# Kernel tuning notes

Hardware: AMD Instinct MI355X
Metric: run time of the kernel (lower is better)

The kernel has to match this reference:

```python
import jax, jax.numpy as jnp
import numpy as np

DEPTH = 256
SEQ = 394
EMB = 300


def _branch(x_nch, W, b, n):
    # W: [depth, n*EMB], flatten order of paragraph[i:i+n,:].flatten() is (time, emb)
    k = W.reshape(DEPTH, n, EMB).transpose(0, 2, 1)  # OIH: [depth, EMB, n]
    y = jax.lax.conv_general_dilated(
        x_nch, k, window_strides=(1,), padding='VALID',
        dimension_numbers=('NCH', 'OIH', 'NCH'))  # [B, depth, SEQ-n+1]
    # original loop only covers windows i = 0 .. SEQ-n-1 (SEQ-n windows)
    y = y[:, :, :SEQ - n] + b  # b: [depth, 1] broadcasts over time
    # running max starts at 0 and relu clamps >= 0; outer relu is a no-op
    return jnp.max(jax.nn.relu(y), axis=-1)  # [B, depth]


def setup_inputs() -> dict:
    key = jax.random.key(0)
    ks = jax.random.split(key, 7)
    inp = {
        'input': jax.random.normal(ks[0], (64, SEQ, EMB), dtype=jnp.float32),
        'W1': jax.random.normal(ks[1], (DEPTH, 3 * EMB), dtype=jnp.float32),
        'W2': jax.random.normal(ks[2], (DEPTH, 4 * EMB), dtype=jnp.float32),
        'W3': jax.random.normal(ks[3], (DEPTH, 5 * EMB), dtype=jnp.float32),
        'b1': jax.random.normal(ks[4], (DEPTH, 1), dtype=jnp.float32),
        'b2': jax.random.normal(ks[5], (DEPTH, 1), dtype=jnp.float32),
        'b3': jax.random.normal(ks[6], (DEPTH, 1), dtype=jnp.float32),
    }
    return inp


def reference(input, W1, W2, W3, b1, b2, b3):
    x = input.transpose(0, 2, 1)  # [B, EMB, SEQ] (NCH)
    o1 = _branch(x, W1, b1, 3)
    o2 = _branch(x, W2, b2, 4)
    o3 = _branch(x, W3, b3, 5)
    return jnp.concatenate([o1, o2, o3], axis=1)  # [B, 3*depth]
```

## Files before the change

kernel.cpp:

```cpp
#include <hip/hip_runtime.h>
#include <hip/hip_bf16.h>

#define SEQ 394
#define EMB 300
#define EMBP 312
#define NROWS (64 * SEQ)
#define NCHT 118
#define CBE0 29
#define CBE1 68
#define XROWS 69
#define XGR 2691
#define XELEM 21528

typedef __attribute__((ext_vector_type(8))) short short8;
typedef __attribute__((ext_vector_type(4))) float f32x4;

__device__ __forceinline__ unsigned short f2b(float f) {
    unsigned u = __float_as_uint(f);
    u += 0x7FFFu + ((u >> 16) & 1u);
    return (unsigned short)(u >> 16);
}


__global__ __launch_bounds__(256)
void pack_w_kernel(const float* __restrict__ W1, const float* __restrict__ W2,
                   const float* __restrict__ W3, unsigned short* __restrict__ wb)
{
    int G = blockIdx.x * 256 + threadIdx.x;
    int l  = G & 63;
    int g  = (G >> 6) & 15;
    int c  = G >> 10;
    const float* Wg; int n, cb;
    if (c <= CBE0)      { Wg = W1; n = 3; cb = 0;        }
    else if (c <= CBE1) { Wg = W2; n = 4; cb = CBE0 + 1; }
    else                { Wg = W3; n = 5; cb = CBE1 + 1; }
    const int K = n * 300;
    const int f = g * 16 + (l & 15);
    const int kl = (c - cb) * 32 + (l >> 4) * 8;
    unsigned short v[8];
#pragma unroll
    for (int j = 0; j < 8; ++j) {
        int kk = kl + j;
        int r  = kk / EMBP;
        int e  = kk - r * EMBP;
        v[j] = (r < n && e < 300) ? f2b(Wg[(long)f * K + r * 300 + e]) : (unsigned short)0;
    }
    unsigned short* dst = wb + (long)G * 8;
    *(ushort4*)dst       = make_ushort4(v[0], v[1], v[2], v[3]);
    *(ushort4*)(dst + 4) = make_ushort4(v[4], v[5], v[6], v[7]);
}


__global__ __launch_bounds__(512, 4)
void convgemm_kernel(const float* __restrict__ x,
                     const unsigned short* __restrict__ wb,
                     const float* __restrict__ b1, const float* __restrict__ b2,
                     const float* __restrict__ b3,
                     float* __restrict__ out)
{
    __shared__ unsigned short X[XELEM];

    const int tid  = threadIdx.x;
    const int lane = tid & 63;
    const int wfs  = tid >> 6;
    const int lr   = lane & 15, lg = lane >> 4;
    const int b    = blockIdx.x >> 3;
    const int ti   = blockIdx.x & 7;
    const int woff = ti * 49;

    const unsigned short* wp0 = wb + ((long)(wfs * 2) * 64 + lane) * 8;
    auto LDW = [&](int c, short8 (&w)[2]) {
        const short8* p = (const short8*)(wp0 + (long)c * 8192);
        w[0] = p[0];
        w[1] = p[64];
    };

    short8 w1[2], w2[2];
    LDW(30, w1); LDW(69, w2);

    {
        const float* xs = x + ((long)b * SEQ + woff) * 300;
        const long growbase = (long)b * SEQ + woff;
#pragma unroll
        for (int rd = 0; rd < 6; ++rd) {
            int gi = rd * 512 + tid;
            if (gi < XGR) {
                int row = gi / 39;
                int g   = gi - row * 39;
                const float* src = xs + (long)gi * 8 - 12 * row;
                float4 v0 = make_float4(0.f, 0.f, 0.f, 0.f);
                float4 v1 = make_float4(0.f, 0.f, 0.f, 0.f);
                if (growbase + row < NROWS) {
                    if (g < 37) {
                        v0 = *(const float4*)src;
                        v1 = *(const float4*)(src + 4);
                    } else if (g == 37) {
                        v0 = *(const float4*)src;
                    }
                }
                short8 s;
                s[0] = (short)f2b(v0.x); s[1] = (short)f2b(v0.y);
                s[2] = (short)f2b(v0.z); s[3] = (short)f2b(v0.w);
                s[4] = (short)f2b(v1.x); s[5] = (short)f2b(v1.y);
                s[6] = (short)f2b(v1.z); s[7] = (short)f2b(v1.w);
                *(short8*)&X[gi * 8] = s;
            }
        }
    }
    __syncthreads();

    const unsigned short* xr = &X[lr * EMBP + lg * 8];
    auto RDBX = [&](int ko, short8 (&bx)[4]) {
        bx[0] = *(const short8*)(xr + ko);
        bx[1] = *(const short8*)(xr + ko + 16 * EMBP);
        bx[2] = *(const short8*)(xr + ko + 32 * EMBP);
        bx[3] = *(const short8*)(xr + ko + 48 * EMBP);
    };

    auto MFMA8 = [&](const short8 (&w)[2], const short8 (&bx)[4], f32x4 (&acc)[2][4]) {
#pragma unroll
        for (int mi = 0; mi < 2; ++mi)
#pragma unroll
            for (int ni = 0; ni < 4; ++ni)
                acc[mi][ni] = __builtin_amdgcn_mfma_f32_16x16x32_bf16(w[mi], bx[ni], acc[mi][ni], 0, 0, 0);
    };

    auto EPI = [&](int br, f32x4 (&acc)[2][4]) {
        const float* bg = (br == 0) ? b1 : (br == 1) ? b2 : b3;
        const int Nw = 391 - br;
        const int ob = b * 768 + br * 256;
#pragma unroll
        for (int mi = 0; mi < 2; ++mi) {
#pragma unroll
            for (int r = 0; r < 4; ++r) {
                const int d = wfs * 32 + mi * 16 + lg * 4 + r;
                const float bv = bg[d];
                float m = 0.f;
#pragma unroll
                for (int ni = 0; ni < 4; ++ni) {
                    int w = woff + ni * 16 + lr;
                    float v = fmaxf(acc[mi][ni][r] + bv, 0.f);
                    if (w >= Nw) v = 0.f;
                    m = fmaxf(m, v);
                }
#pragma unroll
                for (int off = 1; off < 16; off <<= 1)
                    m = fmaxf(m, __shfl_xor(m, off));
                if (lr == 0)
                    atomicMax((int*)(out + ob + d), __float_as_int(m));
            }
        }
#pragma unroll
        for (int i = 0; i < 2; ++i)
#pragma unroll
            for (int j = 0; j < 4; ++j)
                acc[i][j] = (f32x4)0.0f;
    };

    f32x4 accA[2][4], accB[2][4];
#pragma unroll
    for (int i = 0; i < 2; ++i)
#pragma unroll
        for (int j = 0; j < 4; ++j) {
            accA[i][j] = (f32x4)0.0f;
            accB[i][j] = (f32x4)0.0f;
        }

    short8 bxA[4], bxB[4];
    RDBX(0, bxA);

    for (int j = 0; j < 38; j += 2) {
        RDBX((j + 1) * 32, bxB);
        MFMA8(w1, bxA, accA);
        MFMA8(w2, bxA, accB);
        LDW(30 + j + 1, w1); LDW(69 + j + 1, w2);

        RDBX((j + 2) * 32, bxA);
        MFMA8(w1, bxB, accA);
        MFMA8(w2, bxB, accB);
        LDW(30 + j + 2, w1); LDW(69 + j + 2, w2);
    }
    MFMA8(w1, bxA, accA);
    MFMA8(w2, bxA, accB);

    LDW(108, w2);
    RDBX(39 * 32, bxB);
    EPI(1, accA);

    for (int u = 0; u < 10; u += 2) {
        RDBX((40 + u) * 32, bxA);
        MFMA8(w2, bxB, accB);
        LDW(109 + u, w2);

        { int t = (41 + u <= 48) ? 41 + u : 48; RDBX(t * 32, bxB); }
        MFMA8(w2, bxA, accB);
        { int t = (110 + u <= 117) ? 110 + u : 117; LDW(t, w2); }
    }

    LDW(0, w1);
    RDBX(0, bxA);
    EPI(2, accB);

    for (int j = 0; j < 30; j += 2) {
        RDBX((j + 1) * 32, bxB);
        MFMA8(w1, bxA, accA);
        LDW(j + 1, w1);

        { int t = (j + 2 <= 29) ? j + 2 : 29; RDBX(t * 32, bxA); }
        MFMA8(w1, bxB, accA);
        { int t = (j + 2 <= 29) ? j + 2 : 29; LDW(t, w1); }
    }
    EPI(0, accA);
}


__device__ __forceinline__ void load_chunk(const float* __restrict__ Wg,
                                           const float* __restrict__ xb,
                                           int K, int dbase, int i0, int k0, int tid,
                                           float4 wv[4], float4 xv[4])
{
#pragma unroll
    for (int i = 0; i < 4; ++i) {
        int fi  = tid + (i << 8);
        int row = fi >> 3;
        int c4  = (fi & 7) << 2;
        int col = k0 + c4;
        if (col < K)
            wv[i] = *(const float4*)(Wg + (long)(dbase + row) * K + col);
        else
            wv[i] = make_float4(0.f, 0.f, 0.f, 0.f);
        int off = (i0 + row) * EMB + col;
        int lim = SEQ * EMB - 4;
        if (off > lim) off = lim;
        xv[i] = *(const float4*)(xb + off);
    }
}

__device__ __forceinline__ void write_chunk(unsigned short (*Wb)[40],
                                            unsigned short (*Xb)[40],
                                            int tid, const float4 wv[4], const float4 xv[4])
{
#pragma unroll
    for (int i = 0; i < 4; ++i) {
        int fi  = tid + (i << 8);
        int row = fi >> 3;
        int c4  = (fi & 7) << 2;
        *(ushort4*)&Wb[row][c4] = make_ushort4(f2b(wv[i].x), f2b(wv[i].y), f2b(wv[i].z), f2b(wv[i].w));
        *(ushort4*)&Xb[row][c4] = make_ushort4(f2b(xv[i].x), f2b(xv[i].y), f2b(xv[i].z), f2b(xv[i].w));
    }
}

__global__ __launch_bounds__(256, 2)
void convmax_fallback(const float* __restrict__ x,
                      const float* __restrict__ W1, const float* __restrict__ W2,
                      const float* __restrict__ W3,
                      const float* __restrict__ b1, const float* __restrict__ b2,
                      const float* __restrict__ b3,
                      float* __restrict__ out)
{
    const int br = blockIdx.z;
    const int K  = (br == 0) ? 900 : (br == 1) ? 1200 : 1500;
    const int Nw = SEQ - 3 - br;
    const float* Wg = (br == 0) ? W1 : (br == 1) ? W2 : W3;
    const float* bg = (br == 0) ? b1 : (br == 1) ? b2 : b3;
    const int b  = blockIdx.x;
    const int mt = blockIdx.y >> 2;
    const int nt = blockIdx.y & 3;
    const int dbase = mt * 128;
    const int i0    = nt * 128;
    const float* xb = x + b * (SEQ * EMB);
    const int nch = (K + 31) >> 5;

    __shared__ unsigned short Wl[2][128][40];
    __shared__ unsigned short Xl[2][128][40];

    const int tid  = threadIdx.x;
    const int lane = tid & 63;
    const int wid  = tid >> 6;
    const int wr = wid >> 1, wc = wid & 1;
    const int lr = lane & 15, lg = lane >> 4;

    f32x4 acc[4][4];
#pragma unroll
    for (int i = 0; i < 4; ++i)
#pragma unroll
        for (int j = 0; j < 4; ++j)
            acc[i][j] = (f32x4)0.0f;

    {
        float4 wv[4], xv[4];
        load_chunk(Wg, xb, K, dbase, i0, 0, tid, wv, xv);
        write_chunk(Wl[0], Xl[0], tid, wv, xv);
    }
    __syncthreads();

    for (int c = 0; c < nch; ++c) {
        const int cur = c & 1;
        float4 wv[4], xv[4];
        const bool pf = (c + 1 < nch);
        if (pf) load_chunk(Wg, xb, K, dbase, i0, (c + 1) << 5, tid, wv, xv);

        short8 af[4], bfr[4];
#pragma unroll
        for (int mi = 0; mi < 4; ++mi)
            af[mi] = *(const short8*)&Wl[cur][wr * 64 + mi * 16 + lr][lg * 8];
#pragma unroll
        for (int ni = 0; ni < 4; ++ni)
            bfr[ni] = *(const short8*)&Xl[cur][wc * 64 + ni * 16 + lr][lg * 8];
#pragma unroll
        for (int mi = 0; mi < 4; ++mi)
#pragma unroll
            for (int ni = 0; ni < 4; ++ni)
                acc[mi][ni] = __builtin_amdgcn_mfma_f32_16x16x32_bf16(af[mi], bfr[ni], acc[mi][ni], 0, 0, 0);

        if (pf) write_chunk(Wl[cur ^ 1], Xl[cur ^ 1], tid, wv, xv);
        __syncthreads();
    }

    const int ob = b * 768 + br * 256;
#pragma unroll
    for (int mi = 0; mi < 4; ++mi) {
#pragma unroll
        for (int rI = 0; rI < 4; ++rI) {
            const int d = dbase + wr * 64 + mi * 16 + lg * 4 + rI;
            const float bv = bg[d];
            float m = 0.f;
#pragma unroll
            for (int ni = 0; ni < 4; ++ni) {
                int win = i0 + wc * 64 + ni * 16 + lr;
                float v = acc[mi][ni][rI] + bv;
                v = fmaxf(v, 0.f);
                if (win >= Nw) v = 0.f;
                m = fmaxf(m, v);
            }
#pragma unroll
            for (int off = 1; off < 16; off <<= 1)
                m = fmaxf(m, __shfl_xor(m, off));
            if (lr == 0)
                atomicMax((int*)(out + ob + d), __float_as_int(m));
        }
    }
}


extern "C" void kernel_launch(void* const* d_in, const int* in_sizes, int n_in,
                              void* d_out, int out_size, void* d_ws, size_t ws_size,
                              hipStream_t stream) {
    const float* x  = (const float*)d_in[0];
    const float* W1 = (const float*)d_in[1];
    const float* W2 = (const float*)d_in[2];
    const float* W3 = (const float*)d_in[3];
    const float* b1 = (const float*)d_in[4];
    const float* b2 = (const float*)d_in[5];
    const float* b3 = (const float*)d_in[6];
    float* out = (float*)d_out;

    hipMemsetAsync(d_out, 0, (size_t)out_size * sizeof(float), stream);

    const size_t need = (size_t)NCHT * 8192 * 2;

    if (ws_size >= need) {
        unsigned short* wbb = (unsigned short*)d_ws;
        pack_w_kernel<<<472, 256, 0, stream>>>(W1, W2, W3, wbb);
        convgemm_kernel<<<512, 512, 0, stream>>>(x, wbb, b1, b2, b3, out);
    } else {
        dim3 grid(64, 8, 3);
        convmax_fallback<<<grid, 256, 0, stream>>>(x, W1, W2, W3, b1, b2, b3, out);
    }
}
```

Measured before the change: 81.25 us.

## Stagger per-wave chunk order and double-buffer weight registers in conv GEMM

Each wavefront now walks the K-chunks in a rotated order (phase offset by wave index), so the four waves in a block read different LDS rows and weight chunks at the same moment. Weights are double-buffered in registers (A/B sets loaded two chunks ahead), and the activation fragments use a single buffer. The goal is to spread LDS bank and L2 traffic across waves and hide global weight-load latency. The cost is more weight registers, fewer activation registers, and a modular index calculation per step. The reduction order changes per wave, which alters floating-point rounding slightly.

```diff
diff --git a/kernel.cpp b/kernel.cpp
--- a/kernel.cpp
+++ b/kernel.cpp
@@ -75,8 +75,15 @@
         w[1] = p[64];
     };
 
-    short8 w1[2], w2[2];
-    LDW(30, w1); LDW(69, w2);
+    short8 w1A[2], w1B[2], w2A[2], w2B[2];
+
+    const int ph1 = wfs * 5;
+    auto W39 = [](int v) { return v < 39 ? v : v - 39; };
+    auto W10 = [](int v) { return v < 10 ? v : v - 10; };
+    auto W30 = [](int v) { return v < 30 ? v : v - 30; };
+
+    LDW(30 + ph1, w1A); LDW(69 + ph1, w2A);
+    { int c1 = W39(ph1 + 1); LDW(30 + c1, w1B); LDW(69 + c1, w2B); }
 
     {
         const float* xs = x + ((long)b * SEQ + woff) * 300;
@@ -110,14 +117,15 @@
     __syncthreads();
 
     const unsigned short* xr = &X[lr * EMBP + lg * 8];
-    auto RDBX = [&](int ko, short8 (&bx)[4]) {
+    short8 bx[4];
+    auto RDBX = [&](int ko) {
         bx[0] = *(const short8*)(xr + ko);
         bx[1] = *(const short8*)(xr + ko + 16 * EMBP);
         bx[2] = *(const short8*)(xr + ko + 32 * EMBP);
         bx[3] = *(const short8*)(xr + ko + 48 * EMBP);
     };
 
-    auto MFMA8 = [&](const short8 (&w)[2], const short8 (&bx)[4], f32x4 (&acc)[2][4]) {
+    auto MFMA8 = [&](const short8 (&w)[2], f32x4 (&acc)[2][4]) {
 #pragma unroll
         for (int mi = 0; mi < 2; ++mi)
 #pragma unroll
@@ -166,49 +174,58 @@
             accB[i][j] = (f32x4)0.0f;
         }
 
-    short8 bxA[4], bxB[4];
-    RDBX(0, bxA);
-
-    for (int j = 0; j < 38; j += 2) {
-        RDBX((j + 1) * 32, bxB);
-        MFMA8(w1, bxA, accA);
-        MFMA8(w2, bxA, accB);
-        LDW(30 + j + 1, w1); LDW(69 + j + 1, w2);
-
-        RDBX((j + 2) * 32, bxA);
-        MFMA8(w1, bxB, accA);
-        MFMA8(w2, bxB, accB);
-        LDW(30 + j + 2, w1); LDW(69 + j + 2, w2);
-    }
-    MFMA8(w1, bxA, accA);
-    MFMA8(w2, bxA, accB);
-
-    LDW(108, w2);
-    RDBX(39 * 32, bxB);
+    for (int t = 0; t < 38; t += 2) {
+        const int cA  = W39(ph1 + t);
+        const int cB  = W39(ph1 + t + 1);
+        const int cA2 = W39(ph1 + t + 2);
+        const int cB2 = W39(ph1 + t + 3);
+        RDBX(cA * 32);
+        MFMA8(w1A, accA); MFMA8(w2A, accB);
+        LDW(30 + cA2, w1A); LDW(69 + cA2, w2A);
+        RDBX(cB * 32);
+        MFMA8(w1B, accA); MFMA8(w2B, accB);
+        LDW(30 + cB2, w1B); LDW(69 + cB2, w2B);
+    }
+    {
+        const int cT = W39(ph1 + 38);
+        RDBX(cT * 32);
+        MFMA8(w1A, accA); MFMA8(w2A, accB);
+    }
+
+    const int ph2 = wfs;
+    LDW(108 + ph2, w2A);
+    { int c1 = W10(ph2 + 1); LDW(108 + c1, w2B); }
     EPI(1, accA);
 
-    for (int u = 0; u < 10; u += 2) {
-        RDBX((40 + u) * 32, bxA);
-        MFMA8(w2, bxB, accB);
-        LDW(109 + u, w2);
-
-        { int t = (41 + u <= 48) ? 41 + u : 48; RDBX(t * 32, bxB); }
-        MFMA8(w2, bxA, accB);
-        { int t = (110 + u <= 117) ? 110 + u : 117; LDW(t, w2); }
-    }
-
-    LDW(0, w1);
-    RDBX(0, bxA);
+    for (int t = 0; t < 10; t += 2) {
+        const int cA  = W10(ph2 + t);
+        const int cB  = W10(ph2 + t + 1);
+        const int cA2 = W10(ph2 + t + 2);
+        const int cB2 = W10(ph2 + t + 3);
+        RDBX((39 + cA) * 32);
+        MFMA8(w2A, accB);
+        LDW(108 + cA2, w2A);
+        RDBX((39 + cB) * 32);
+        MFMA8(w2B, accB);
+        LDW(108 + cB2, w2B);
+    }
+
+    const int ph0 = wfs * 4;
+    LDW(ph0, w1A);
+    { int c1 = W30(ph0 + 1); LDW(c1, w1B); }
     EPI(2, accB);
 
-    for (int j = 0; j < 30; j += 2) {
-        RDBX((j + 1) * 32, bxB);
-        MFMA8(w1, bxA, accA);
-        LDW(j + 1, w1);
-
-        { int t = (j + 2 <= 29) ? j + 2 : 29; RDBX(t * 32, bxA); }
-        MFMA8(w1, bxB, accA);
-        { int t = (j + 2 <= 29) ? j + 2 : 29; LDW(t, w1); }
+    for (int t = 0; t < 30; t += 2) {
+        const int cA  = W30(ph0 + t);
+        const int cB  = W30(ph0 + t + 1);
+        const int cA2 = W30(ph0 + t + 2);
+        const int cB2 = W30(ph0 + t + 3);
+        RDBX(cA * 32);
+        MFMA8(w1A, accA);
+        LDW(cA2, w1A);
+        RDBX(cB * 32);
+        MFMA8(w1B, accA);
+        LDW(cB2, w1B);
     }
     EPI(0, accA);
 }
```

Measured after the change: 82.88 us. About the same (+2.0%).

## Tile over flattened batch-sequence rows with 112-row blocks spanning batches

Applied to the files above, without the earlier changes.

Replaces the per-batch tiling (8 tiles of 49 windows per batch, 512 blocks) with tiles of 112 consecutive flattened rows (226 blocks), each wave computing 7 N-subtiles instead of 4. The intent is to raise weight reuse per MFMA, since each loaded weight fragment now feeds 14 MFMAs, and to cut the redundant halo rows and weight traffic that per-batch tiles incurred. The epilogue now splits each tile's max between two batches when a tile crosses a batch boundary. The costs are more accumulator registers (occupancy hint lowered to 2), more LDS per block, and fewer blocks than CUs, which may leave the GPU underfilled.

```diff
diff --git a/kernel.cpp b/kernel.cpp
--- a/kernel.cpp
+++ b/kernel.cpp
@@ -8,9 +8,12 @@
 #define NCHT 118
 #define CBE0 29
 #define CBE1 68
-#define XROWS 69
-#define XGR 2691
-#define XELEM 21528
+#define RPB 112
+#define NBLK 226
+#define XROWS 116
+#define XGR 4524
+#define XELEM 36192
+#define NISTR 4992
 
 typedef __attribute__((ext_vector_type(8))) short short8;
 typedef __attribute__((ext_vector_type(4))) float f32x4;
@@ -51,7 +54,7 @@
 }
 
 
-__global__ __launch_bounds__(512, 4)
+__global__ __launch_bounds__(512, 2)
 void convgemm_kernel(const float* __restrict__ x,
                      const unsigned short* __restrict__ wb,
                      const float* __restrict__ b1, const float* __restrict__ b2,
@@ -64,9 +67,7 @@
     const int lane = tid & 63;
     const int wfs  = tid >> 6;
     const int lr   = lane & 15, lg = lane >> 4;
-    const int b    = blockIdx.x >> 3;
-    const int ti   = blockIdx.x & 7;
-    const int woff = ti * 49;
+    const long r0  = (long)blockIdx.x * RPB;
 
     const unsigned short* wp0 = wb + ((long)(wfs * 2) * 64 + lane) * 8;
     auto LDW = [&](int c, short8 (&w)[2]) {
@@ -79,10 +80,9 @@
     LDW(30, w1); LDW(69, w2);
 
     {
-        const float* xs = x + ((long)b * SEQ + woff) * 300;
-        const long growbase = (long)b * SEQ + woff;
-#pragma unroll
-        for (int rd = 0; rd < 6; ++rd) {
+        const float* xs = x + r0 * 300;
+#pragma unroll
+        for (int rd = 0; rd < 9; ++rd) {
             int gi = rd * 512 + tid;
             if (gi < XGR) {
                 int row = gi / 39;
@@ -90,7 +90,7 @@
                 const float* src = xs + (long)gi * 8 - 12 * row;
                 float4 v0 = make_float4(0.f, 0.f, 0.f, 0.f);
                 float4 v1 = make_float4(0.f, 0.f, 0.f, 0.f);
-                if (growbase + row < NROWS) {
+                if (r0 + row < NROWS) {
                     if (g < 37) {
                         v0 = *(const float4*)src;
                         v1 = *(const float4*)(src + 4);
@@ -110,78 +110,88 @@
     __syncthreads();
 
     const unsigned short* xr = &X[lr * EMBP + lg * 8];
-    auto RDBX = [&](int ko, short8 (&bx)[4]) {
-        bx[0] = *(const short8*)(xr + ko);
-        bx[1] = *(const short8*)(xr + ko + 16 * EMBP);
-        bx[2] = *(const short8*)(xr + ko + 32 * EMBP);
-        bx[3] = *(const short8*)(xr + ko + 48 * EMBP);
+    auto RDBX = [&](int ko, short8 (&bx)[7]) {
+#pragma unroll
+        for (int ni = 0; ni < 7; ++ni)
+            bx[ni] = *(const short8*)(xr + ko + ni * NISTR);
     };
 
-    auto MFMA8 = [&](const short8 (&w)[2], const short8 (&bx)[4], f32x4 (&acc)[2][4]) {
+    auto MFMA14 = [&](const short8 (&w)[2], const short8 (&bx)[7], f32x4 (&acc)[2][7]) {
 #pragma unroll
         for (int mi = 0; mi < 2; ++mi)
 #pragma unroll
-            for (int ni = 0; ni < 4; ++ni)
+            for (int ni = 0; ni < 7; ++ni)
                 acc[mi][ni] = __builtin_amdgcn_mfma_f32_16x16x32_bf16(w[mi], bx[ni], acc[mi][ni], 0, 0, 0);
     };
 
-    auto EPI = [&](int br, f32x4 (&acc)[2][4]) {
+    const int  B0  = (int)(r0 / SEQ);
+    const long rB1 = (long)(B0 + 1) * SEQ;
+    const bool cross = (r0 + RPB - 1) >= rB1;
+
+    auto EPI = [&](int br, f32x4 (&acc)[2][7]) {
         const float* bg = (br == 0) ? b1 : (br == 1) ? b2 : b3;
         const int Nw = 391 - br;
-        const int ob = b * 768 + br * 256;
 #pragma unroll
         for (int mi = 0; mi < 2; ++mi) {
 #pragma unroll
             for (int r = 0; r < 4; ++r) {
                 const int d = wfs * 32 + mi * 16 + lg * 4 + r;
                 const float bv = bg[d];
-                float m = 0.f;
-#pragma unroll
-                for (int ni = 0; ni < 4; ++ni) {
-                    int w = woff + ni * 16 + lr;
+                float vlo = 0.f, vhi = 0.f;
+#pragma unroll
+                for (int ni = 0; ni < 7; ++ni) {
+                    long rr = r0 + ni * 16 + lr;
+                    bool hi = rr >= rB1;
+                    long ii = rr - (hi ? rB1 : (long)B0 * SEQ);
                     float v = fmaxf(acc[mi][ni][r] + bv, 0.f);
-                    if (w >= Nw) v = 0.f;
-                    m = fmaxf(m, v);
+                    if (ii >= Nw || (hi && B0 + 1 >= 64)) v = 0.f;
+                    vlo = hi ? vlo : fmaxf(vlo, v);
+                    vhi = hi ? fmaxf(vhi, v) : vhi;
                 }
 #pragma unroll
-                for (int off = 1; off < 16; off <<= 1)
-                    m = fmaxf(m, __shfl_xor(m, off));
-                if (lr == 0)
-                    atomicMax((int*)(out + ob + d), __float_as_int(m));
+                for (int off = 1; off < 16; off <<= 1) {
+                    vlo = fmaxf(vlo, __shfl_xor(vlo, off));
+                    vhi = fmaxf(vhi, __shfl_xor(vhi, off));
+                }
+                if (lr == 0) {
+                    atomicMax((int*)(out + (long)B0 * 768 + br * 256 + d), __float_as_int(vlo));
+                    if (cross && B0 + 1 < 64)
+                        atomicMax((int*)(out + (long)(B0 + 1) * 768 + br * 256 + d), __float_as_int(vhi));
+                }
             }
         }
 #pragma unroll
         for (int i = 0; i < 2; ++i)
 #pragma unroll
-            for (int j = 0; j < 4; ++j)
+            for (int j = 0; j < 7; ++j)
                 acc[i][j] = (f32x4)0.0f;
     };
 
-    f32x4 accA[2][4], accB[2][4];
+    f32x4 accA[2][7], accB[2][7];
 #pragma unroll
     for (int i = 0; i < 2; ++i)
 #pragma unroll
-        for (int j = 0; j < 4; ++j) {
+        for (int j = 0; j < 7; ++j) {
             accA[i][j] = (f32x4)0.0f;
             accB[i][j] = (f32x4)0.0f;
         }
 
-    short8 bxA[4], bxB[4];
+    short8 bxA[7], bxB[7];
     RDBX(0, bxA);
 
     for (int j = 0; j < 38; j += 2) {
         RDBX((j + 1) * 32, bxB);
-        MFMA8(w1, bxA, accA);
-        MFMA8(w2, bxA, accB);
+        MFMA14(w1, bxA, accA);
+        MFMA14(w2, bxA, accB);
         LDW(30 + j + 1, w1); LDW(69 + j + 1, w2);
 
         RDBX((j + 2) * 32, bxA);
-        MFMA8(w1, bxB, accA);
-        MFMA8(w2, bxB, accB);
+        MFMA14(w1, bxB, accA);
+        MFMA14(w2, bxB, accB);
         LDW(30 + j + 2, w1); LDW(69 + j + 2, w2);
     }
-    MFMA8(w1, bxA, accA);
-    MFMA8(w2, bxA, accB);
+    MFMA14(w1, bxA, accA);
+    MFMA14(w2, bxA, accB);
 
     LDW(108, w2);
     RDBX(39 * 32, bxB);
@@ -189,11 +199,11 @@
 
     for (int u = 0; u < 10; u += 2) {
         RDBX((40 + u) * 32, bxA);
-        MFMA8(w2, bxB, accB);
+        MFMA14(w2, bxB, accB);
         LDW(109 + u, w2);
 
         { int t = (41 + u <= 48) ? 41 + u : 48; RDBX(t * 32, bxB); }
-        MFMA8(w2, bxA, accB);
+        MFMA14(w2, bxA, accB);
         { int t = (110 + u <= 117) ? 110 + u : 117; LDW(t, w2); }
     }
 
@@ -203,11 +213,11 @@
 
     for (int j = 0; j < 30; j += 2) {
         RDBX((j + 1) * 32, bxB);
-        MFMA8(w1, bxA, accA);
+        MFMA14(w1, bxA, accA);
         LDW(j + 1, w1);
 
         { int t = (j + 2 <= 29) ? j + 2 : 29; RDBX(t * 32, bxA); }
-        MFMA8(w1, bxB, accA);
+        MFMA14(w1, bxB, accA);
         { int t = (j + 2 <= 29) ? j + 2 : 29; LDW(t, w1); }
     }
     EPI(0, accA);
@@ -362,7 +372,7 @@
     if (ws_size >= need) {
         unsigned short* wbb = (unsigned short*)d_ws;
         pack_w_kernel<<<472, 256, 0, stream>>>(W1, W2, W3, wbb);
-        convgemm_kernel<<<512, 512, 0, stream>>>(x, wbb, b1, b2, b3, out);
+        convgemm_kernel<<<NBLK, 512, 0, stream>>>(x, wbb, b1, b2, b3, out);
     } else {
         dim3 grid(64, 8, 3);
         convmax_fallback<<<grid, 256, 0, stream>>>(x, W1, W2, W3, b1, b2, b3, out);
```

Result: no change. 79.84 us (-1.7%).

## Tile conv GEMM over flattened rows with 1024-thread blocks spanning batches

Applied to the files above, without the earlier changes.

Replaces the per-batch 8-way window tiling (512 blocks of 512 threads, 49 windows plus halo each) with a flat tiling over batch*SEQ rows: 197 blocks of 1024 threads, each covering 128 rows. Two wave halves share each weight fragment, which raises weight reuse per block, and the flat tiling reduces redundant halo loads. The epilogue now splits the max between two batches when a tile straddles a batch boundary. In exchange, 197 blocks at one block per CU leave some of the 256 CUs idle and lower occupancy, and the larger shared-memory footprint limits concurrency.

```diff
diff --git a/kernel.cpp b/kernel.cpp
--- a/kernel.cpp
+++ b/kernel.cpp
@@ -8,9 +8,11 @@
 #define NCHT 118
 #define CBE0 29
 #define CBE1 68
-#define XROWS 69
-#define XGR 2691
-#define XELEM 21528
+#define RPB 128
+#define NBLK 197
+#define XROWS 132
+#define XGR 5148
+#define XELEM 41184
 
 typedef __attribute__((ext_vector_type(8))) short short8;
 typedef __attribute__((ext_vector_type(4))) float f32x4;
@@ -51,7 +53,7 @@
 }
 
 
-__global__ __launch_bounds__(512, 4)
+__global__ __launch_bounds__(1024, 1)
 void convgemm_kernel(const float* __restrict__ x,
                      const unsigned short* __restrict__ wb,
                      const float* __restrict__ b1, const float* __restrict__ b2,
@@ -62,11 +64,11 @@
 
     const int tid  = threadIdx.x;
     const int lane = tid & 63;
-    const int wfs  = tid >> 6;
+    const int wid  = tid >> 6;
+    const int wfs  = wid >> 1;
+    const int ws   = wid & 1;
     const int lr   = lane & 15, lg = lane >> 4;
-    const int b    = blockIdx.x >> 3;
-    const int ti   = blockIdx.x & 7;
-    const int woff = ti * 49;
+    const long r0  = (long)blockIdx.x * RPB;
 
     const unsigned short* wp0 = wb + ((long)(wfs * 2) * 64 + lane) * 8;
     auto LDW = [&](int c, short8 (&w)[2]) {
@@ -79,18 +81,17 @@
     LDW(30, w1); LDW(69, w2);
 
     {
-        const float* xs = x + ((long)b * SEQ + woff) * 300;
-        const long growbase = (long)b * SEQ + woff;
+        const float* xs = x + r0 * 300;
 #pragma unroll
         for (int rd = 0; rd < 6; ++rd) {
-            int gi = rd * 512 + tid;
+            int gi = rd * 1024 + tid;
             if (gi < XGR) {
                 int row = gi / 39;
                 int g   = gi - row * 39;
                 const float* src = xs + (long)gi * 8 - 12 * row;
                 float4 v0 = make_float4(0.f, 0.f, 0.f, 0.f);
                 float4 v1 = make_float4(0.f, 0.f, 0.f, 0.f);
-                if (growbase + row < NROWS) {
+                if (r0 + row < NROWS) {
                     if (g < 37) {
                         v0 = *(const float4*)src;
                         v1 = *(const float4*)(src + 4);
@@ -109,7 +110,7 @@
     }
     __syncthreads();
 
-    const unsigned short* xr = &X[lr * EMBP + lg * 8];
+    const unsigned short* xr = &X[(ws * 64 + lr) * EMBP + lg * 8];
     auto RDBX = [&](int ko, short8 (&bx)[4]) {
         bx[0] = *(const short8*)(xr + ko);
         bx[1] = *(const short8*)(xr + ko + 16 * EMBP);
@@ -125,29 +126,40 @@
                 acc[mi][ni] = __builtin_amdgcn_mfma_f32_16x16x32_bf16(w[mi], bx[ni], acc[mi][ni], 0, 0, 0);
     };
 
+    const int  B0  = (int)(r0 / SEQ);
+    const long rB1 = (long)(B0 + 1) * SEQ;
+    const bool cross = (r0 + RPB - 1) >= rB1;
+
     auto EPI = [&](int br, f32x4 (&acc)[2][4]) {
         const float* bg = (br == 0) ? b1 : (br == 1) ? b2 : b3;
         const int Nw = 391 - br;
-        const int ob = b * 768 + br * 256;
 #pragma unroll
         for (int mi = 0; mi < 2; ++mi) {
 #pragma unroll
             for (int r = 0; r < 4; ++r) {
                 const int d = wfs * 32 + mi * 16 + lg * 4 + r;
                 const float bv = bg[d];
-                float m = 0.f;
+                float vlo = 0.f, vhi = 0.f;
 #pragma unroll
                 for (int ni = 0; ni < 4; ++ni) {
-                    int w = woff + ni * 16 + lr;
+                    long rr = r0 + ws * 64 + ni * 16 + lr;
+                    bool hi = rr >= rB1;
+                    long ii = rr - (hi ? rB1 : (long)B0 * SEQ);
                     float v = fmaxf(acc[mi][ni][r] + bv, 0.f);
-                    if (w >= Nw) v = 0.f;
-                    m = fmaxf(m, v);
+                    if (ii >= Nw) v = 0.f;
+                    vlo = hi ? vlo : fmaxf(vlo, v);
+                    vhi = hi ? fmaxf(vhi, v) : vhi;
                 }
 #pragma unroll
-                for (int off = 1; off < 16; off <<= 1)
-                    m = fmaxf(m, __shfl_xor(m, off));
-                if (lr == 0)
-                    atomicMax((int*)(out + ob + d), __float_as_int(m));
+                for (int off = 1; off < 16; off <<= 1) {
+                    vlo = fmaxf(vlo, __shfl_xor(vlo, off));
+                    vhi = fmaxf(vhi, __shfl_xor(vhi, off));
+                }
+                if (lr == 0) {
+                    atomicMax((int*)(out + (long)B0 * 768 + br * 256 + d), __float_as_int(vlo));
+                    if (cross && B0 + 1 < 64)
+                        atomicMax((int*)(out + (long)(B0 + 1) * 768 + br * 256 + d), __float_as_int(vhi));
+                }
             }
         }
 #pragma unroll
@@ -362,7 +374,7 @@
     if (ws_size >= need) {
         unsigned short* wbb = (unsigned short*)d_ws;
         pack_w_kernel<<<472, 256, 0, stream>>>(W1, W2, W3, wbb);
-        convgemm_kernel<<<512, 512, 0, stream>>>(x, wbb, b1, b2, b3, out);
+        convgemm_kernel<<<NBLK, 1024, 0, stream>>>(x, wbb, b1, b2, b3, out);
     } else {
         dim3 grid(64, 8, 3);
         convmax_fallback<<<grid, 256, 0, stream>>>(x, W1, W2, W3, b1, b2, b3, out);
```

After: 76.40 us. 6.0% less time.
